# Performance work log

Hardware: AMD Instinct MI355X
Metric: run time of the kernel (lower is better)

## Reference

```python
import jax, jax.numpy as jnp
import numpy as np
from jax import lax

# pywt db8 decomposition low-pass filter (dec_lo), 16 taps
DB8_DEC_LO = jnp.array([
    -0.00011747678400228192, 0.0006754494059985568, -0.0003917403729959771,
    -0.00487035299301066, 0.008746094047015655, 0.013981027917015516,
    -0.04408825393106472, -0.01736930100202211, 0.128747426620186,
    0.00047248457399797254, -0.2840155429624281, -0.015829105256023893,
    0.5853546836548691, 0.6756307362980128, 0.3128715909144659,
    0.05441584224308161], dtype=jnp.float32)

FLEN = 16


def dwt2_ll(x):
    """LL band of pywt.dwt2(x, 'db8', mode='symmetric') for x [B,C,H,W].
    pywt dwt along an axis == symmetric pad by flen-1, full correlation with
    reversed dec_lo, take every other sample starting at offset 1."""
    B, C, H, W = x.shape
    f = DB8_DEC_LO[::-1]  # np.convolve flips the filter -> correlate with reversed
    xr = x.reshape(B * C, 1, H, W)
    # along W
    p = jnp.pad(xr, ((0, 0), (0, 0), (0, 0), (FLEN - 1, FLEN - 1)), mode='symmetric')[..., 1:]
    y = lax.conv_general_dilated(p, f.reshape(1, 1, 1, FLEN), (1, 2), 'VALID',
                                 dimension_numbers=('NCHW', 'OIHW', 'NCHW'))
    # along H
    p = jnp.pad(y, ((0, 0), (0, 0), (FLEN - 1, FLEN - 1), (0, 0)), mode='symmetric')[:, :, 1:, :]
    z = lax.conv_general_dilated(p, f.reshape(1, 1, FLEN, 1), (2, 1), 'VALID',
                                 dimension_numbers=('NCHW', 'OIHW', 'NCHW'))
    return z.reshape(B, C, z.shape[2], z.shape[3])


def setup_inputs() -> dict:
    key = jax.random.key(0)
    k1, k2, k3, k4 = jax.random.split(key, 4)
    B, C, H, W = 8, 128, 256, 256
    r = 16
    x = jax.random.normal(k1, (B, C, H, W), jnp.float32)
    conv_w = jax.random.normal(k2, (1, 2, 7, 7), jnp.float32) * 0.1  # SpatialAttention conv, no bias
    fc_w1 = jax.random.normal(k3, (C // r, C), jnp.float32) * (1.0 / np.sqrt(C))
    fc_w2 = jax.random.normal(k4, (C, C // r), jnp.float32) * (1.0 / np.sqrt(C // r))
    weight = jnp.array(0.0, dtype=jnp.float32)  # learnable fusion scalar
    return {"x": x, "conv_w": conv_w, "fc_w1": fc_w1, "fc_w2": fc_w2, "weight": weight}


def reference(x, conv_w, fc_w1, fc_w2, weight):
    # --- spatial attention ---
    avg = jnp.mean(x, axis=1, keepdims=True)
    mx = jnp.max(x, axis=1, keepdims=True)
    s = jnp.concatenate([avg, mx], axis=1)  # [B,2,H,W]
    attn = jax.nn.sigmoid(lax.conv_general_dilated(
        s, conv_w, (1, 1), ((3, 3), (3, 3)),
        dimension_numbers=('NCHW', 'OIHW', 'NCHW')))  # [B,1,H,W]
    spatial_out = x * attn
    # --- wavelet (frequency) attention; LL detached in the original ---
    ll = lax.stop_gradient(dwt2_ll(x))  # [B,C,H',W']
    y = jnp.mean(ll, axis=(2, 3))  # global avg pool -> [B,C]
    h = jax.nn.relu(y @ fc_w1.T)
    w = jax.nn.sigmoid(h @ fc_w2.T)[:, :, None, None]  # [B,C,1,1]
    wavelet_out = x * w
    # --- gated fusion ---
    alpha = jax.nn.sigmoid(weight)
    out = alpha * spatial_out + (1.0 - alpha) * wavelet_out
    return out, attn, w, alpha
```

## Files before the change

kernel.cpp:

```cpp
#include <hip/hip_runtime.h>
#include <math.h>

#define BB 8
#define CC 128
#define HH 256
#define WW 256
#define HWD 65536
#define NOUT (67108864)

#define ATTN_OFF ((size_t)NOUT)
#define W_OFF (ATTN_OFF + (size_t)BB * HWD)
#define ALPHA_OFF (W_OFF + (size_t)BB * CC)

__constant__ float g_declo[16] = {
    -0.00011747678400228192f, 0.0006754494059985568f, -0.0003917403729959771f,
    -0.00487035299301066f,    0.008746094047015655f,  0.013981027917015516f,
    -0.04408825393106472f,    -0.01736930100202211f,  0.128747426620186f,
    0.00047248457399797254f,  -0.2840155429624281f,   -0.015829105256023893f,
    0.5853546836548691f,      0.6756307362980128f,    0.3128715909144659f,
    0.05441584224308161f};

__device__ __forceinline__ float sigmoidf_(float v) {
    return 1.0f / (1.0f + expf(-v));
}

__global__ void compute_a_kernel(float* __restrict__ a_arr) {
    int t = threadIdx.x;
    float acc = 0.0f;
    for (int j = 0; j < 135; ++j) {
        for (int k = 0; k < 16; ++k) {
            int idx = 2 * j + k - 14;
            int s = (idx < 0) ? (-1 - idx) : ((idx >= WW) ? (511 - idx) : idx);
            if (s == t) acc += g_declo[15 - k];
        }
    }
    a_arr[t] = acc;
}

__global__ __launch_bounds__(256) void pass1_kernel(
    const float* __restrict__ x, const float* __restrict__ a_arr,
    float* __restrict__ avg_s, float* __restrict__ max_s,
    float* __restrict__ partial) {
    const int blk = blockIdx.x;
    const int b = blk >> 8;
    const int h = blk & 255;
    const int tid = threadIdx.x;
    const int wv = tid >> 6;
    const int lane = tid & 63;

    __shared__ float dotc[CC];
    __shared__ __align__(16) float lsum[4][256];
    __shared__ __align__(16) float lmax[4][256];

    const float4 a4 = reinterpret_cast<const float4*>(a_arr)[lane];
    const float ah = a_arr[h];

    float4 sum4 = {0.f, 0.f, 0.f, 0.f};
    float4 max4 = {-INFINITY, -INFINITY, -INFINITY, -INFINITY};

    const size_t base = (size_t)b * CC * HWD + (size_t)h * WW;
    for (int ccc = 0; ccc < 32; ++ccc) {
        const int c = wv * 32 + ccc;
        const float4 v =
            reinterpret_cast<const float4*>(x + base + (size_t)c * HWD)[lane];
        float dot = a4.x * v.x + a4.y * v.y + a4.z * v.z + a4.w * v.w;
#pragma unroll
        for (int off = 32; off >= 1; off >>= 1)
            dot += __shfl_down(dot, off, 64);
        if (lane == 0) dotc[c] = dot;
        sum4.x += v.x; sum4.y += v.y; sum4.z += v.z; sum4.w += v.w;
        max4.x = fmaxf(max4.x, v.x); max4.y = fmaxf(max4.y, v.y);
        max4.z = fmaxf(max4.z, v.z); max4.w = fmaxf(max4.w, v.w);
    }
    reinterpret_cast<float4*>(&lsum[wv][0])[lane] = sum4;
    reinterpret_cast<float4*>(&lmax[wv][0])[lane] = max4;
    __syncthreads();

    const int col = tid;
    float s = lsum[0][col] + lsum[1][col] + lsum[2][col] + lsum[3][col];
    float m = fmaxf(fmaxf(lmax[0][col], lmax[1][col]),
                    fmaxf(lmax[2][col], lmax[3][col]));
    const size_t po = (size_t)b * HWD + (size_t)h * WW + col;
    avg_s[po] = s * (1.0f / 128.0f);
    max_s[po] = m;
    if (tid < CC) partial[(size_t)blk * CC + tid] = dotc[tid] * ah;
}

__global__ __launch_bounds__(128) void mlp_kernel(
    const float* __restrict__ partial, const float* __restrict__ fc_w1,
    const float* __restrict__ fc_w2, const float* __restrict__ weight,
    float* __restrict__ w_out, float* __restrict__ alpha_out) {
    const int b = blockIdx.x;
    const int c = threadIdx.x;
    float acc = 0.0f;
    for (int h = 0; h < HH; ++h)
        acc += partial[((size_t)(b * HH + h)) * CC + c];
    const float y = acc * (1.0f / (135.0f * 135.0f));

    __shared__ float ysh[CC];
    __shared__ float hsh[8];
    ysh[c] = y;
    __syncthreads();
    if (c < 8) {
        float ha = 0.0f;
        for (int k = 0; k < CC; ++k) ha += ysh[k] * fc_w1[c * CC + k];
        hsh[c] = fmaxf(ha, 0.0f);
    }
    __syncthreads();
    float wa = 0.0f;
#pragma unroll
    for (int i = 0; i < 8; ++i) wa += hsh[i] * fc_w2[c * 8 + i];
    w_out[b * CC + c] = sigmoidf_(wa);
    if (b == 0 && c == 0) alpha_out[0] = sigmoidf_(weight[0]);
}

__global__ __launch_bounds__(256) void conv_attn_kernel(
    const float* __restrict__ avg_s, const float* __restrict__ max_s,
    const float* __restrict__ cw, float* __restrict__ attn_out) {
    const int blk = blockIdx.x;
    const int b = blk >> 8;
    const int h = blk & 255;
    const int w = threadIdx.x;

    __shared__ float k0[49], k1[49];
    if (threadIdx.x < 49) {
        k0[threadIdx.x] = cw[threadIdx.x];
        k1[threadIdx.x] = cw[49 + threadIdx.x];
    }
    __syncthreads();

    const float* A = avg_s + (size_t)b * HWD;
    const float* M = max_s + (size_t)b * HWD;
    float acc = 0.0f;
    for (int kh = 0; kh < 7; ++kh) {
        const int ih = h + kh - 3;
        if (ih < 0 || ih >= HH) continue;
        for (int kw = 0; kw < 7; ++kw) {
            const int iw = w + kw - 3;
            if (iw < 0 || iw >= WW) continue;
            const float a = A[ih * WW + iw];
            const float m = M[ih * WW + iw];
            acc = fmaf(k0[kh * 7 + kw], a, acc);
            acc = fmaf(k1[kh * 7 + kw], m, acc);
        }
    }
    attn_out[(size_t)b * HWD + (size_t)h * WW + w] = sigmoidf_(acc);
}

__global__ __launch_bounds__(256) void final_mix_kernel(
    const float* __restrict__ x, const float* __restrict__ attn,
    const float* __restrict__ wvec, const float* __restrict__ weight,
    float* __restrict__ out) {
    const size_t i4 = (size_t)blockIdx.x * 256 + threadIdx.x;
    const size_t flat = i4 * 4;
    const int b = (int)(flat >> 23);
    const int rem = (int)(flat & ((1u << 23) - 1));
    const int c = rem >> 16;
    const int hw = rem & (HWD - 1);

    const float alpha = sigmoidf_(weight[0]);
    const float wc = (1.0f - alpha) * wvec[b * CC + c];

    const float4 x4 = reinterpret_cast<const float4*>(x)[i4];
    const float4 a4 =
        *reinterpret_cast<const float4*>(attn + (size_t)b * HWD + hw);
    float4 o;
    o.x = x4.x * fmaf(alpha, a4.x, wc);
    o.y = x4.y * fmaf(alpha, a4.y, wc);
    o.z = x4.z * fmaf(alpha, a4.z, wc);
    o.w = x4.w * fmaf(alpha, a4.w, wc);
    reinterpret_cast<float4*>(out)[i4] = o;
}

extern "C" void kernel_launch(void* const* d_in, const int* in_sizes, int n_in,
                              void* d_out, int out_size, void* d_ws,
                              size_t ws_size, hipStream_t stream) {
    const float* x = (const float*)d_in[0];
    const float* conv_w = (const float*)d_in[1];
    const float* fc_w1 = (const float*)d_in[2];
    const float* fc_w2 = (const float*)d_in[3];
    const float* weight = (const float*)d_in[4];

    float* out = (float*)d_out;
    float* attn_out = out + ATTN_OFF;
    float* w_out = out + W_OFF;
    float* alpha_out = out + ALPHA_OFF;

    float* wsf = (float*)d_ws;
    float* a_arr = wsf;
    float* avg_s = wsf + 256;
    float* max_s = avg_s + (size_t)BB * HWD;
    float* partial = max_s + (size_t)BB * HWD;

    compute_a_kernel<<<1, 256, 0, stream>>>(a_arr);
    pass1_kernel<<<BB * HH, 256, 0, stream>>>(x, a_arr, avg_s, max_s, partial);
    mlp_kernel<<<BB, 128, 0, stream>>>(partial, fc_w1, fc_w2, weight, w_out,
                                       alpha_out);
    conv_attn_kernel<<<BB * HH, 256, 0, stream>>>(avg_s, max_s, conv_w,
                                                  attn_out);
    final_mix_kernel<<<NOUT / 4 / 256, 256, 0, stream>>>(x, attn_out, w_out,
                                                         weight, out);
}
```

Measured before the change: 556.4 us.

## Fuse conv attention with final mix, inline filter weights, batch dot reductions

Folds the 7x7 spatial-attention conv into the final mixing kernel, staging the avg/max rows in shared memory. This removes a separate launch and the re-read of the attention map from global memory. Filter weights are now computed in closed form inside pass1, dropping the compute_a launch. Per-channel dot reductions are batched through a shared-memory transpose instead of one shuffle chain per channel, and the MLP reduction is spread over 1024 threads. The fused kernel reads x row by row across channels, a different access pattern from the earlier flat streaming pass.

Result: faster. 543.0 us (-2.4%).

```diff
diff --git a/kernel.cpp b/kernel.cpp
--- a/kernel.cpp
+++ b/kernel.cpp
@@ -24,23 +24,21 @@
     return 1.0f / (1.0f + expf(-v));
 }
 
-__global__ void compute_a_kernel(float* __restrict__ a_arr) {
-    int t = threadIdx.x;
-    float acc = 0.0f;
-    for (int j = 0; j < 135; ++j) {
-        for (int k = 0; k < 16; ++k) {
-            int idx = 2 * j + k - 14;
-            int s = (idx < 0) ? (-1 - idx) : ((idx >= WW) ? (511 - idx) : idx);
-            if (s == t) acc += g_declo[15 - k];
-        }
-    }
-    a_arr[t] = acc;
+__device__ __forceinline__ float a_weight(int t) {
+    float v = 0.0f;
+    for (int k = (t & 1); k < 16; k += 2) v += g_declo[15 - k];
+    if (t <= 13) {
+        for (int k = 13 - t; k >= 0; k -= 2) v += g_declo[15 - k];
+    }
+    if (t >= 242) {
+        for (int k = 257 - t; k < 16; k += 2) v += g_declo[15 - k];
+    }
+    return v;
 }
 
 __global__ __launch_bounds__(256) void pass1_kernel(
-    const float* __restrict__ x, const float* __restrict__ a_arr,
-    float* __restrict__ avg_s, float* __restrict__ max_s,
-    float* __restrict__ partial) {
+    const float* __restrict__ x, float* __restrict__ avg_s,
+    float* __restrict__ max_s, float* __restrict__ partial) {
     const int blk = blockIdx.x;
     const int b = blk >> 8;
     const int h = blk & 255;
@@ -48,128 +46,173 @@
     const int wv = tid >> 6;
     const int lane = tid & 63;
 
+    __shared__ __align__(16) float a_sh[256];
     __shared__ float dotc[CC];
     __shared__ __align__(16) float lsum[4][256];
     __shared__ __align__(16) float lmax[4][256];
-
-    const float4 a4 = reinterpret_cast<const float4*>(a_arr)[lane];
-    const float ah = a_arr[h];
+    __shared__ float T[4][64][17];
+
+    a_sh[tid] = a_weight(tid);
+    __syncthreads();
+
+    const float4 a4 = reinterpret_cast<const float4*>(a_sh)[lane];
+    const float ah = a_sh[h];
 
     float4 sum4 = {0.f, 0.f, 0.f, 0.f};
     float4 max4 = {-INFINITY, -INFINITY, -INFINITY, -INFINITY};
 
-    const size_t base = (size_t)b * CC * HWD + (size_t)h * WW;
-    for (int ccc = 0; ccc < 32; ++ccc) {
-        const int c = wv * 32 + ccc;
-        const float4 v =
-            reinterpret_cast<const float4*>(x + base + (size_t)c * HWD)[lane];
-        float dot = a4.x * v.x + a4.y * v.y + a4.z * v.z + a4.w * v.w;
-#pragma unroll
-        for (int off = 32; off >= 1; off >>= 1)
-            dot += __shfl_down(dot, off, 64);
-        if (lane == 0) dotc[c] = dot;
-        sum4.x += v.x; sum4.y += v.y; sum4.z += v.z; sum4.w += v.w;
-        max4.x = fmaxf(max4.x, v.x); max4.y = fmaxf(max4.y, v.y);
-        max4.z = fmaxf(max4.z, v.z); max4.w = fmaxf(max4.w, v.w);
-    }
+    const size_t base = (size_t)b * CC * HWD + (size_t)h * WW + (lane << 2);
+
+    for (int g = 0; g < 2; ++g) {
+        const int cbase = (wv << 5) + (g << 4);
+        float dots[16];
+#pragma unroll
+        for (int i = 0; i < 16; ++i) {
+            const float4 v = *reinterpret_cast<const float4*>(
+                x + base + (size_t)(cbase + i) * HWD);
+            dots[i] = a4.x * v.x + a4.y * v.y + a4.z * v.z + a4.w * v.w;
+            sum4.x += v.x; sum4.y += v.y; sum4.z += v.z; sum4.w += v.w;
+            max4.x = fmaxf(max4.x, v.x); max4.y = fmaxf(max4.y, v.y);
+            max4.z = fmaxf(max4.z, v.z); max4.w = fmaxf(max4.w, v.w);
+        }
+#pragma unroll
+        for (int i = 0; i < 16; ++i) T[wv][lane][i] = dots[i];
+        const int cr = lane & 15;
+        const int q = lane >> 4;
+        float s = 0.f;
+#pragma unroll
+        for (int j = 0; j < 16; ++j) s += T[wv][(q << 4) + j][cr];
+        s += __shfl_xor(s, 16, 64);
+        s += __shfl_xor(s, 32, 64);
+        if (lane < 16) dotc[cbase + lane] = s;
+    }
+
     reinterpret_cast<float4*>(&lsum[wv][0])[lane] = sum4;
     reinterpret_cast<float4*>(&lmax[wv][0])[lane] = max4;
     __syncthreads();
 
     const int col = tid;
-    float s = lsum[0][col] + lsum[1][col] + lsum[2][col] + lsum[3][col];
-    float m = fmaxf(fmaxf(lmax[0][col], lmax[1][col]),
-                    fmaxf(lmax[2][col], lmax[3][col]));
+    const float s = lsum[0][col] + lsum[1][col] + lsum[2][col] + lsum[3][col];
+    const float m = fmaxf(fmaxf(lmax[0][col], lmax[1][col]),
+                          fmaxf(lmax[2][col], lmax[3][col]));
     const size_t po = (size_t)b * HWD + (size_t)h * WW + col;
     avg_s[po] = s * (1.0f / 128.0f);
     max_s[po] = m;
     if (tid < CC) partial[(size_t)blk * CC + tid] = dotc[tid] * ah;
 }
 
-__global__ __launch_bounds__(128) void mlp_kernel(
+__global__ __launch_bounds__(1024) void mlp_kernel(
     const float* __restrict__ partial, const float* __restrict__ fc_w1,
     const float* __restrict__ fc_w2, const float* __restrict__ weight,
     float* __restrict__ w_out, float* __restrict__ alpha_out) {
     const int b = blockIdx.x;
-    const int c = threadIdx.x;
+    const int t = threadIdx.x;
+    const int c = t & 127;
+    const int g = t >> 7;
+
     float acc = 0.0f;
-    for (int h = 0; h < HH; ++h)
+    for (int h = g; h < HH; h += 8)
         acc += partial[((size_t)(b * HH + h)) * CC + c];
-    const float y = acc * (1.0f / (135.0f * 135.0f));
-
+
+    __shared__ float red[8][CC];
     __shared__ float ysh[CC];
     __shared__ float hsh[8];
-    ysh[c] = y;
-    __syncthreads();
-    if (c < 8) {
+    red[g][c] = acc;
+    __syncthreads();
+
+    if (t < CC) {
+        float y = 0.0f;
+#pragma unroll
+        for (int i = 0; i < 8; ++i) y += red[i][t];
+        ysh[t] = y * (1.0f / (135.0f * 135.0f));
+    }
+    __syncthreads();
+    if (t < 8) {
         float ha = 0.0f;
-        for (int k = 0; k < CC; ++k) ha += ysh[k] * fc_w1[c * CC + k];
-        hsh[c] = fmaxf(ha, 0.0f);
-    }
-    __syncthreads();
-    float wa = 0.0f;
-#pragma unroll
-    for (int i = 0; i < 8; ++i) wa += hsh[i] * fc_w2[c * 8 + i];
-    w_out[b * CC + c] = sigmoidf_(wa);
-    if (b == 0 && c == 0) alpha_out[0] = sigmoidf_(weight[0]);
-}
-
-__global__ __launch_bounds__(256) void conv_attn_kernel(
-    const float* __restrict__ avg_s, const float* __restrict__ max_s,
-    const float* __restrict__ cw, float* __restrict__ attn_out) {
+        for (int k = 0; k < CC; ++k) ha += ysh[k] * fc_w1[t * CC + k];
+        hsh[t] = fmaxf(ha, 0.0f);
+    }
+    __syncthreads();
+    if (t < CC) {
+        float wa = 0.0f;
+#pragma unroll
+        for (int i = 0; i < 8; ++i) wa += hsh[i] * fc_w2[t * 8 + i];
+        w_out[b * CC + t] = sigmoidf_(wa);
+    }
+    if (b == 0 && t == 0) alpha_out[0] = sigmoidf_(weight[0]);
+}
+
+__global__ __launch_bounds__(256) void conv_mix_kernel(
+    const float* __restrict__ x, const float* __restrict__ avg_s,
+    const float* __restrict__ max_s, const float* __restrict__ cw,
+    const float* __restrict__ wvec, const float* __restrict__ alpha_p,
+    float* __restrict__ attn_out, float* __restrict__ out) {
     const int blk = blockIdx.x;
     const int b = blk >> 8;
     const int h = blk & 255;
-    const int w = threadIdx.x;
+    const int tid = threadIdx.x;
+    const int wv = tid >> 6;
+    const int lane = tid & 63;
 
     __shared__ float k0[49], k1[49];
-    if (threadIdx.x < 49) {
-        k0[threadIdx.x] = cw[threadIdx.x];
-        k1[threadIdx.x] = cw[49 + threadIdx.x];
-    }
-    __syncthreads();
-
-    const float* A = avg_s + (size_t)b * HWD;
-    const float* M = max_s + (size_t)b * HWD;
+    __shared__ __align__(16) float sA[7][256];
+    __shared__ __align__(16) float sM[7][256];
+    __shared__ __align__(16) float att[256];
+    __shared__ float wrow[CC];
+
+    if (tid < 49) {
+        k0[tid] = cw[tid];
+        k1[tid] = cw[49 + tid];
+    }
+    if (tid < CC) wrow[tid] = wvec[b * CC + tid];
+
+#pragma unroll
+    for (int r = 0; r < 7; ++r) {
+        const int ih = h - 3 + r;
+        if (ih >= 0 && ih < HH) {
+            sA[r][tid] = avg_s[(size_t)b * HWD + ih * WW + tid];
+            sM[r][tid] = max_s[(size_t)b * HWD + ih * WW + tid];
+        }
+    }
+    __syncthreads();
+
     float acc = 0.0f;
-    for (int kh = 0; kh < 7; ++kh) {
-        const int ih = h + kh - 3;
+#pragma unroll
+    for (int r = 0; r < 7; ++r) {
+        const int ih = h - 3 + r;
         if (ih < 0 || ih >= HH) continue;
+#pragma unroll
         for (int kw = 0; kw < 7; ++kw) {
-            const int iw = w + kw - 3;
+            const int iw = tid + kw - 3;
             if (iw < 0 || iw >= WW) continue;
-            const float a = A[ih * WW + iw];
-            const float m = M[ih * WW + iw];
-            acc = fmaf(k0[kh * 7 + kw], a, acc);
-            acc = fmaf(k1[kh * 7 + kw], m, acc);
+            acc = fmaf(k0[r * 7 + kw], sA[r][iw], acc);
+            acc = fmaf(k1[r * 7 + kw], sM[r][iw], acc);
         }
     }
-    attn_out[(size_t)b * HWD + (size_t)h * WW + w] = sigmoidf_(acc);
-}
-
-__global__ __launch_bounds__(256) void final_mix_kernel(
-    const float* __restrict__ x, const float* __restrict__ attn,
-    const float* __restrict__ wvec, const float* __restrict__ weight,
-    float* __restrict__ out) {
-    const size_t i4 = (size_t)blockIdx.x * 256 + threadIdx.x;
-    const size_t flat = i4 * 4;
-    const int b = (int)(flat >> 23);
-    const int rem = (int)(flat & ((1u << 23) - 1));
-    const int c = rem >> 16;
-    const int hw = rem & (HWD - 1);
-
-    const float alpha = sigmoidf_(weight[0]);
-    const float wc = (1.0f - alpha) * wvec[b * CC + c];
-
-    const float4 x4 = reinterpret_cast<const float4*>(x)[i4];
-    const float4 a4 =
-        *reinterpret_cast<const float4*>(attn + (size_t)b * HWD + hw);
-    float4 o;
-    o.x = x4.x * fmaf(alpha, a4.x, wc);
-    o.y = x4.y * fmaf(alpha, a4.y, wc);
-    o.z = x4.z * fmaf(alpha, a4.z, wc);
-    o.w = x4.w * fmaf(alpha, a4.w, wc);
-    reinterpret_cast<float4*>(out)[i4] = o;
+    const float av = sigmoidf_(acc);
+    attn_out[(size_t)b * HWD + h * WW + tid] = av;
+    att[tid] = av;
+    __syncthreads();
+
+    const float alpha = alpha_p[0];
+    const float one_m = 1.0f - alpha;
+    const float4 at4 = reinterpret_cast<const float4*>(att)[lane];
+    const float4 aa4 = {alpha * at4.x, alpha * at4.y, alpha * at4.z,
+                        alpha * at4.w};
+    const size_t rowbase = (size_t)b * CC * HWD + (size_t)h * WW + (lane << 2);
+#pragma unroll 4
+    for (int ci = 0; ci < 32; ++ci) {
+        const int c = (wv << 5) + ci;
+        const float wc = one_m * wrow[c];
+        const float4 x4 =
+            *reinterpret_cast<const float4*>(x + rowbase + (size_t)c * HWD);
+        float4 o;
+        o.x = x4.x * (aa4.x + wc);
+        o.y = x4.y * (aa4.y + wc);
+        o.z = x4.z * (aa4.z + wc);
+        o.w = x4.w * (aa4.w + wc);
+        *reinterpret_cast<float4*>(out + rowbase + (size_t)c * HWD) = o;
+    }
 }
 
 extern "C" void kernel_launch(void* const* d_in, const int* in_sizes, int n_in,
@@ -187,17 +230,14 @@
     float* alpha_out = out + ALPHA_OFF;
 
     float* wsf = (float*)d_ws;
-    float* a_arr = wsf;
-    float* avg_s = wsf + 256;
+    float* avg_s = wsf;
     float* max_s = avg_s + (size_t)BB * HWD;
     float* partial = max_s + (size_t)BB * HWD;
 
-    compute_a_kernel<<<1, 256, 0, stream>>>(a_arr);
-    pass1_kernel<<<BB * HH, 256, 0, stream>>>(x, a_arr, avg_s, max_s, partial);
-    mlp_kernel<<<BB, 128, 0, stream>>>(partial, fc_w1, fc_w2, weight, w_out,
-                                       alpha_out);
-    conv_attn_kernel<<<BB * HH, 256, 0, stream>>>(avg_s, max_s, conv_w,
-                                                  attn_out);
-    final_mix_kernel<<<NOUT / 4 / 256, 256, 0, stream>>>(x, attn_out, w_out,
-                                                         weight, out);
-}
+    pass1_kernel<<<BB * HH, 256, 0, stream>>>(x, avg_s, max_s, partial);
+    mlp_kernel<<<BB, 1024, 0, stream>>>(partial, fc_w1, fc_w2, weight, w_out,
+                                        alpha_out);
+    conv_mix_kernel<<<BB * HH, 256, 0, stream>>>(x, avg_s, max_s, conv_w,
+                                                 w_out, alpha_out, attn_out,
+                                                 out);
+}
```
